# Kernel optimization log

Hardware: AMD Instinct MI355X
Metric: run time of the kernel (lower is better)

Reference implementation:

```python
import jax, jax.numpy as jnp
import numpy as np

NEG_SLOPE = 0.2  # PyG GATv2Conv default leaky_relu negative slope


def _gatv2_layer(x, src, dst, n, Wl, bl, Wr, br, att, bias, concat):
    # PyG GATv2Conv (share_weights=False, edge_dim=None):
    #   x_l = lin_l(x) on source, x_r = lin_r(x) on target
    #   m = leaky_relu(x_l[src] + x_r[dst]); alpha = softmax_dst(<m, att>)
    #   out[i] = sum_{e: dst=i} alpha_e * x_l[src_e]
    H, C = att.shape
    xl = (x @ Wl + bl).reshape(n, H, C)
    xr = (x @ Wr + br).reshape(n, H, C)
    m = jax.nn.leaky_relu(xl[src] + xr[dst], NEG_SLOPE)      # [E,H,C]
    logits = jnp.einsum('ehc,hc->eh', m, att)                # [E,H]
    lmax = jax.ops.segment_max(logits, dst, num_segments=n)  # [N,H]
    e = jnp.exp(logits - lmax[dst])
    denom = jax.ops.segment_sum(e, dst, num_segments=n)
    alpha = e / (denom[dst] + 1e-16)                         # [E,H]
    out = jax.ops.segment_sum(xl[src] * alpha[:, :, None], dst, num_segments=n)
    out = out.reshape(n, H * C) if concat else out.mean(axis=1)
    return out + bias


def _glorot(key, shape):
    fan_in, fan_out = shape[0], shape[-1]
    s = jnp.sqrt(6.0 / (fan_in + fan_out))
    return jax.random.uniform(key, shape, jnp.float32, -s, s)


def setup_inputs() -> dict:
    key = jax.random.key(0)
    N, E, B = 50000, 800000, 512
    node_in, hidden, heads, meta_dim = 128, 32, 4, 12
    ks = jax.random.split(key, 32)
    inp = {
        'x': jax.random.normal(ks[0], (N, node_in), jnp.float32),
        'edge_index': jax.random.randint(ks[1], (2, E), 0, N, jnp.int64),
        'batch': jnp.sort(jax.random.randint(ks[2], (N,), 0, B, jnp.int64)),
        'metadata': jax.random.normal(ks[3], (B, meta_dim), jnp.float32),
    }
    dims = [(node_in, hidden, heads), (hidden * heads, hidden, heads), (hidden * heads, hidden, 1)]
    i = 4
    for li, (din, dh, H) in enumerate(dims):
        inp[f'Wl{li}'] = _glorot(ks[i], (din, H * dh)); i += 1
        inp[f'bl{li}'] = jnp.zeros((H * dh,), jnp.float32)
        inp[f'Wr{li}'] = _glorot(ks[i], (din, H * dh)); i += 1
        inp[f'br{li}'] = jnp.zeros((H * dh,), jnp.float32)
        inp[f'att{li}'] = _glorot(ks[i], (H, dh)); i += 1
        out_dim = H * dh if li < 2 else dh  # last layer concat=False
        inp[f'b{li}'] = jnp.zeros((out_dim,), jnp.float32)
    pool_dim = hidden  # n_layers=3 -> final single-head layer
    inp['Wh1'] = _glorot(ks[i], (pool_dim + meta_dim, pool_dim)); i += 1
    inp['bh1'] = jnp.zeros((pool_dim,), jnp.float32)
    inp['Wh2'] = _glorot(ks[i], (pool_dim, 1)); i += 1
    inp['bh2'] = jnp.zeros((1,), jnp.float32)
    return inp


def reference(x, edge_index, batch, metadata,
              Wl0, bl0, Wr0, br0, att0, b0,
              Wl1, bl1, Wr1, br1, att1, b1,
              Wl2, bl2, Wr2, br2, att2, b2,
              Wh1, bh1, Wh2, bh2):
    n = x.shape[0]
    B = metadata.shape[0]
    # PyG GATv2Conv add_self_loops=True
    loop = jnp.arange(n, dtype=edge_index.dtype)
    src = jnp.concatenate([edge_index[0], loop])
    dst = jnp.concatenate([edge_index[1], loop])
    params = [(Wl0, bl0, Wr0, br0, att0, b0, True),
              (Wl1, bl1, Wr1, br1, att1, b1, True),
              (Wl2, bl2, Wr2, br2, att2, b2, False)]
    h = x
    for (Wl, bl, Wr, br, att, bias, concat) in params:
        h = _gatv2_layer(h, src, dst, n, Wl, bl, Wr, br, att, bias, concat)
        h = jax.nn.elu(h)  # dropout is identity in eval mode
    # global mean pool over graphs
    sums = jax.ops.segment_sum(h, batch, num_segments=B)
    cnt = jax.ops.segment_sum(jnp.ones((n,), h.dtype), batch, num_segments=B)
    emb = sums / jnp.clip(cnt, 1.0)[:, None]
    z = jnp.concatenate([emb, metadata], axis=1)
    z = jax.nn.relu(z @ Wh1 + bh1)
    return z @ Wh2 + bh2  # (B, 1) logits
```

## Files before the change

### kernel.cpp

```cpp
#include <hip/hip_runtime.h>
#include <cstdint>
#include <cstddef>

#define NEG_SLOPE 0.2f
#define LOG2E 1.44269504f

typedef __attribute__((ext_vector_type(8))) short short8;
typedef __attribute__((ext_vector_type(4))) float f32x4;

__device__ __forceinline__ float bf2f(unsigned short u) {
    union { unsigned int i; float f; } x; x.i = ((unsigned int)u) << 16; return x.f;
}
__device__ __forceinline__ unsigned short f2bf(float f) {
    union { float f; unsigned int i; } x;
    x.f = f;
    unsigned int u = x.i;
    return (unsigned short)((u + 0x7FFFu + ((u >> 16) & 1u)) >> 16);
}

__device__ __forceinline__ float dpp_sum8(float p) {
    p += __int_as_float(__builtin_amdgcn_update_dpp(0, __float_as_int(p), 0xB1, 0xF, 0xF, true));
    p += __int_as_float(__builtin_amdgcn_update_dpp(0, __float_as_int(p), 0x4E, 0xF, 0xF, true));
    p += __int_as_float(__builtin_amdgcn_update_dpp(0, __float_as_int(p), 0x141, 0xF, 0xF, true));
    return p;
}

__global__ __launch_bounds__(256) void prep_w_all(
    const float* __restrict__ Wl0, const float* __restrict__ Wr0,
    const float* __restrict__ Wl1, const float* __restrict__ Wr1,
    const float* __restrict__ Wl2, const float* __restrict__ Wr2,
    unsigned short* __restrict__ Bt0, unsigned short* __restrict__ Bt1,
    unsigned short* __restrict__ Bt2)
{
    int idx = blockIdx.x * 256 + threadIdx.x;
    const int SZ = 256 * 128;
    const float *Wl, *Wr; unsigned short* Bt; int dout;
    if (idx < SZ)              { Wl = Wl0; Wr = Wr0; Bt = Bt0; dout = 128; }
    else if (idx < 2 * SZ)     { Wl = Wl1; Wr = Wr1; Bt = Bt1; dout = 128; idx -= SZ; }
    else if (idx < 2 * SZ + 64 * 128) { Wl = Wl2; Wr = Wr2; Bt = Bt2; dout = 32; idx -= 2 * SZ; }
    else return;
    int n = idx >> 7, k = idx & 127;
    float v = (n < dout) ? Wl[(size_t)k * dout + n] : Wr[(size_t)k * dout + (n - dout)];
    Bt[idx] = f2bf(v);
}

template<int BN, bool ABF16>
__global__ __launch_bounds__(256) void gemm_mfma(
    const void* __restrict__ Avoid, int M,
    const unsigned short* __restrict__ Bt,
    const float* __restrict__ bl, const float* __restrict__ br,
    int dout, unsigned short* __restrict__ XL, unsigned short* __restrict__ XR)
{
    constexpr int LDA = 136;
    constexpr int NT  = BN / 16;
    __shared__ __attribute__((aligned(16))) unsigned short As[64 * LDA];
    __shared__ __attribute__((aligned(16))) unsigned short Bs[BN * LDA];
    const int t  = threadIdx.x;
    const int m0 = blockIdx.x * 64;
    const int n0 = blockIdx.y * BN;

    if (ABF16) {
        const unsigned short* A = (const unsigned short*)Avoid;
#pragma unroll
        for (int i = 0; i < 8; ++i) {
            int c   = t + i * 256;
            int row = c >> 5;
            int col = (c & 31) * 4;
            int gr  = m0 + row;
            ushort4 v = make_ushort4(0, 0, 0, 0);
            if (gr < M) v = *(const ushort4*)(A + (size_t)gr * 128 + col);
            *(ushort4*)(As + row * LDA + col) = v;
        }
    } else {
        const float* A = (const float*)Avoid;
#pragma unroll
        for (int i = 0; i < 8; ++i) {
            int c   = t + i * 256;
            int row = c >> 5;
            int col = (c & 31) * 4;
            int gr  = m0 + row;
            float4 v = make_float4(0.f, 0.f, 0.f, 0.f);
            if (gr < M) v = *(const float4*)(A + (size_t)gr * 128 + col);
            ushort4 o;
            o.x = f2bf(v.x); o.y = f2bf(v.y); o.z = f2bf(v.z); o.w = f2bf(v.w);
            *(ushort4*)(As + row * LDA + col) = o;
        }
    }
#pragma unroll
    for (int i = 0; i < BN / 16; ++i) {
        int c  = t + i * 256;
        int n  = c >> 4;
        int kc = (c & 15) * 8;
        *(short8*)(Bs + n * LDA + kc) =
            *(const short8*)(Bt + (size_t)(n0 + n) * 128 + kc);
    }
    __syncthreads();

    const int w    = t >> 6;
    const int lane = t & 63;
    const int fr   = lane & 15;
    const int quad = lane >> 4;

    f32x4 acc[NT] = {};
    const unsigned short* ap = As + (w * 16 + fr) * LDA + quad * 8;
    const unsigned short* bp = Bs + fr * LDA + quad * 8;
#pragma unroll
    for (int k0 = 0; k0 < 128; k0 += 32) {
        short8 afr = *(const short8*)(ap + k0);
#pragma unroll
        for (int j = 0; j < NT; ++j) {
            short8 bfr = *(const short8*)(bp + j * 16 * LDA + k0);
            acc[j] = __builtin_amdgcn_mfma_f32_16x16x32_bf16(afr, bfr, acc[j], 0, 0, 0);
        }
    }

#pragma unroll
    for (int j = 0; j < NT; ++j) {
        int col = n0 + j * 16 + fr;
        float bias = (col < dout) ? bl[col] : br[col - dout];
#pragma unroll
        for (int r = 0; r < 4; ++r) {
            int row = m0 + w * 16 + quad * 4 + r;
            if (row < M) {
                unsigned short o = f2bf(acc[j][r] + bias);
                if (col < dout) XL[(size_t)row * dout + col] = o;
                else            XR[(size_t)row * dout + (col - dout)] = o;
            }
        }
    }
}

__global__ void count_rank_kernel(const int* __restrict__ dst, int E,
                                  int* __restrict__ cnt, unsigned short* __restrict__ rank)
{
    int e = blockIdx.x * blockDim.x + threadIdx.x;
    if (e < E) {
        int p = atomicAdd(&cnt[dst[e]], 1);
        rank[e] = (unsigned short)p;
    }
}

__global__ __launch_bounds__(256) void scan_partial(
    const int* __restrict__ cnt, int N, int* __restrict__ bsum)
{
    __shared__ int red[4];
    const int t = threadIdx.x;
    const int base = blockIdx.x * 2048;
    int s = 0;
#pragma unroll
    for (int i = 0; i < 8; ++i) {
        int idx = base + t + i * 256;
        if (idx < N) s += cnt[idx];
    }
#pragma unroll
    for (int off = 32; off >= 1; off >>= 1) s += __shfl_xor(s, off);
    if ((t & 63) == 0) red[t >> 6] = s;
    __syncthreads();
    if (t == 0) bsum[blockIdx.x] = red[0] + red[1] + red[2] + red[3];
}

__global__ __launch_bounds__(256) void scan_bsums(
    int* __restrict__ bsum, int nb, int E, int* __restrict__ rowptr, int N)
{
    __shared__ int sh[256];
    const int t = threadIdx.x;
    int v = (t < nb) ? bsum[t] : 0;
    sh[t] = v;
    __syncthreads();
    for (int off = 1; off < 256; off <<= 1) {
        int u = (t >= off) ? sh[t - off] : 0;
        __syncthreads();
        sh[t] += u;
        __syncthreads();
    }
    if (t < nb) bsum[t] = sh[t] - v;
    if (t == 0) rowptr[N] = E;
}

__global__ __launch_bounds__(256) void scan_final(
    const int* __restrict__ cnt, int N, const int* __restrict__ bsum,
    int* __restrict__ rowptr)
{
    __shared__ int sdat[2048];
    __shared__ int tsum[256];
    const int t = threadIdx.x;
    const int base = blockIdx.x * 2048;
#pragma unroll
    for (int i = 0; i < 8; ++i) {
        int idx = base + t + i * 256;
        sdat[t + i * 256] = (idx < N) ? cnt[idx] : 0;
    }
    __syncthreads();
    int vals[8];
    int s = 0;
#pragma unroll
    for (int j = 0; j < 8; ++j) { vals[j] = sdat[t * 8 + j]; s += vals[j]; }
    tsum[t] = s;
    __syncthreads();
    for (int off = 1; off < 256; off <<= 1) {
        int u = (t >= off) ? tsum[t - off] : 0;
        __syncthreads();
        tsum[t] += u;
        __syncthreads();
    }
    int run = bsum[blockIdx.x] + tsum[t] - s;
#pragma unroll
    for (int j = 0; j < 8; ++j) { sdat[t * 8 + j] = run; run += vals[j]; }
    __syncthreads();
#pragma unroll
    for (int i = 0; i < 8; ++i) {
        int idx = base + t + i * 256;
        if (idx < N) rowptr[idx] = sdat[t + i * 256];
    }
}

__global__ void place_kernel(const int* __restrict__ src, const int* __restrict__ dst,
                             const unsigned short* __restrict__ rank, int E,
                             const int* __restrict__ rowptr,
                             unsigned short* __restrict__ csr_src)
{
    int e = blockIdx.x * blockDim.x + threadIdx.x;
    if (e < E)
        csr_src[rowptr[dst[e]] + rank[e]] = (unsigned short)src[e];
}

template<int H>
__global__ __launch_bounds__(256, 4) void gat_fused(
    const unsigned short* __restrict__ xl, const unsigned short* __restrict__ xr,
    const int* __restrict__ rowptr, const unsigned short* __restrict__ csr_src,
    const float* __restrict__ att, const float* __restrict__ bias,
    unsigned short* __restrict__ hout, int hstride, int N)
{
    constexpr int HC  = 32 * H;
    constexpr int LPE = HC / 4;
    constexpr int EPW = 64 / LPE;
    const int node = blockIdx.x * 4 + (threadIdx.x >> 6);
    if (node >= N) return;
    const int lane = threadIdx.x & 63;
    const int q    = lane % LPE;
    const int slot = lane / LPE;
    const int rs   = rowptr[node];
    const int re   = rowptr[node + 1];

    const unsigned short* __restrict__ xlb = xl + 4 * q;
    float4 xri;
    {
        ushort4 u = *(const ushort4*)(xr + (size_t)node * HC + 4 * q);
        xri.x = bf2f(u.x); xri.y = bf2f(u.y); xri.z = bf2f(u.z); xri.w = bf2f(u.w);
    }
    float4 af = *(const float4*)(att + 4 * q);
    af.x *= LOG2E; af.y *= LOG2E; af.z *= LOG2E; af.w *= LOG2E;

    float l = 0.f;
    float4 acc = make_float4(0.f, 0.f, 0.f, 0.f);

    auto ld4 = [&](int s) -> float4 {
        ushort4 u = *(const ushort4*)(xlb + (size_t)s * HC);
        float4 v;
        v.x = bf2f(u.x); v.y = bf2f(u.y); v.z = bf2f(u.z); v.w = bf2f(u.w);
        return v;
    };

    auto edge_w = [&](const float4& v) -> float {
        float sx = v.x + xri.x, sy = v.y + xri.y, sz = v.z + xri.z, sw = v.w + xri.w;
        sx = fmaxf(sx, NEG_SLOPE * sx);
        sy = fmaxf(sy, NEG_SLOPE * sy);
        sz = fmaxf(sz, NEG_SLOPE * sz);
        sw = fmaxf(sw, NEG_SLOPE * sw);
        float p = af.x * sx;
        p = fmaf(af.y, sy, p);
        p = fmaf(af.z, sz, p);
        p = fmaf(af.w, sw, p);
        p = dpp_sum8(p);
        return exp2f(p);
    };

    if (slot == 0) {
        float4 v = ld4(node);
        float w = edge_w(v);
        l = w;
        acc.x = w * v.x; acc.y = w * v.y; acc.z = w * v.z; acc.w = w * v.w;
    }

    int k = rs + slot;
    for (; k + EPW < re; k += 2 * EPW) {
        int s0 = csr_src[k];
        int s1 = csr_src[k + EPW];
        float4 v0 = ld4(s0);
        float4 v1 = ld4(s1);
        float w0 = edge_w(v0);
        float w1 = edge_w(v1);
        l += w0 + w1;
        acc.x = fmaf(w0, v0.x, fmaf(w1, v1.x, acc.x));
        acc.y = fmaf(w0, v0.y, fmaf(w1, v1.y, acc.y));
        acc.z = fmaf(w0, v0.z, fmaf(w1, v1.z, acc.z));
        acc.w = fmaf(w0, v0.w, fmaf(w1, v1.w, acc.w));
    }
    if (k < re) {
        int s0 = csr_src[k];
        float4 v0 = ld4(s0);
        float w0 = edge_w(v0);
        l += w0;
        acc.x = fmaf(w0, v0.x, acc.x);
        acc.y = fmaf(w0, v0.y, acc.y);
        acc.z = fmaf(w0, v0.z, acc.z);
        acc.w = fmaf(w0, v0.w, acc.w);
    }

#pragma unroll
    for (int mask = LPE; mask < 64; mask <<= 1) {
        l     += __shfl_xor(l, mask);
        acc.x += __shfl_xor(acc.x, mask);
        acc.y += __shfl_xor(acc.y, mask);
        acc.z += __shfl_xor(acc.z, mask);
        acc.w += __shfl_xor(acc.w, mask);
    }

    if (lane < LPE) {
        const float4 bi = *(const float4*)(bias + 4 * q);
        float inv = 1.f / (l + 1e-16f);
        float4 o;
        o.x = acc.x * inv + bi.x;
        o.y = acc.y * inv + bi.y;
        o.z = acc.z * inv + bi.z;
        o.w = acc.w * inv + bi.w;
        o.x = (o.x > 0.f) ? o.x : expm1f(o.x);
        o.y = (o.y > 0.f) ? o.y : expm1f(o.y);
        o.z = (o.z > 0.f) ? o.z : expm1f(o.z);
        o.w = (o.w > 0.f) ? o.w : expm1f(o.w);
        ushort4 ob;
        ob.x = f2bf(o.x); ob.y = f2bf(o.y); ob.z = f2bf(o.z); ob.w = f2bf(o.w);
        *(ushort4*)(hout + (size_t)node * hstride + 4 * q) = ob;
    }
}

__global__ __launch_bounds__(128) void pool_head_kernel(
    const unsigned short* __restrict__ h, int hstride,
    const int* __restrict__ batch, int N,
    const float* __restrict__ meta,
    const float* __restrict__ Wh1, const float* __restrict__ bh1,
    const float* __restrict__ Wh2, const float* __restrict__ bh2,
    float* __restrict__ out)
{
    const int b = blockIdx.x;
    const int t = threadIdx.x;
    __shared__ float s[128];
    __shared__ float z[44];

    int lo = 0, hi = N;
    while (lo < hi) { int mid = (lo + hi) >> 1; if (batch[mid] < b) lo = mid + 1; else hi = mid; }
    int lo2 = lo, hi2 = N;
    while (lo2 < hi2) { int mid = (lo2 + hi2) >> 1; if (batch[mid] < b + 1) lo2 = mid + 1; else hi2 = mid; }
    const int start = lo, end = lo2;

    const int c = t & 31, r = t >> 5;
    float acc = 0.f;
    for (int row = start + r; row < end; row += 4)
        acc += bf2f(h[(size_t)row * hstride + c]);
    s[t] = acc;
    __syncthreads();
    if (t < 32) {
        float sum = s[t] + s[t + 32] + s[t + 64] + s[t + 96];
        z[t] = sum / fmaxf((float)(end - start), 1.0f);
    } else if (t < 44) {
        z[t] = meta[(size_t)b * 12 + (t - 32)];
    }
    __syncthreads();
    if (t < 32) {
        float hj = bh1[t];
#pragma unroll
        for (int k = 0; k < 44; ++k)
            hj = fmaf(z[k], Wh1[k * 32 + t], hj);
        hj = fmaxf(hj, 0.f);
        float p = hj * Wh2[t];
#pragma unroll
        for (int off = 16; off >= 1; off >>= 1)
            p += __shfl_xor(p, off, 32);
        if (t == 0) out[b] = p + bh2[0];
    }
}

extern "C" void kernel_launch(void* const* d_in, const int* in_sizes, int n_in,
                              void* d_out, int out_size, void* d_ws, size_t ws_size,
                              hipStream_t stream)
{
    const float* x     = (const float*)d_in[0];
    const int*   ei    = (const int*)d_in[1];
    const int*   batch = (const int*)d_in[2];
    const float* meta  = (const float*)d_in[3];
    const float* Wl[3]  = {(const float*)d_in[4],  (const float*)d_in[10], (const float*)d_in[16]};
    const float* bl[3]  = {(const float*)d_in[5],  (const float*)d_in[11], (const float*)d_in[17]};
    const float* Wr[3]  = {(const float*)d_in[6],  (const float*)d_in[12], (const float*)d_in[18]};
    const float* br[3]  = {(const float*)d_in[7],  (const float*)d_in[13], (const float*)d_in[19]};
    const float* att[3] = {(const float*)d_in[8],  (const float*)d_in[14], (const float*)d_in[20]};
    const float* bb[3]  = {(const float*)d_in[9],  (const float*)d_in[15], (const float*)d_in[21]};
    const float* Wh1 = (const float*)d_in[22];
    const float* bh1 = (const float*)d_in[23];
    const float* Wh2 = (const float*)d_in[24];
    const float* bh2 = (const float*)d_in[25];
    float* out = (float*)d_out;

    const int N  = in_sizes[0] / 128;
    const int E  = in_sizes[1] / 2;
    const int B  = in_sizes[3] / 12;
    const int NB = (N + 2047) / 2048;

    char* wsp = (char*)d_ws;
    size_t off_ = 0;
    auto alloc = [&](size_t bytes) {
        char* p = wsp + off_;
        off_ = (off_ + bytes + 255) & ~(size_t)255;
        return p;
    };
    unsigned short* xlbuf = (unsigned short*)alloc((size_t)N * 128 * 2);
    unsigned short* xrbuf = (unsigned short*)alloc((size_t)N * 128 * 2);
    unsigned short* hbuf  = (unsigned short*)alloc((size_t)N * 128 * 2);
    int*   cnt     = (int*)alloc((size_t)N * 4);
    int*   rowptr  = (int*)alloc((size_t)(N + 1) * 4);
    unsigned short* rank    = (unsigned short*)alloc((size_t)E * 2);
    unsigned short* csr_src = (unsigned short*)alloc((size_t)E * 2);
    unsigned short* Bt0     = (unsigned short*)alloc((size_t)256 * 128 * 2);
    unsigned short* Bt1     = (unsigned short*)alloc((size_t)256 * 128 * 2);
    unsigned short* Bt2     = (unsigned short*)alloc((size_t)64 * 128 * 2);
    int*   bsum    = (int*)alloc((size_t)256 * 4);

    const int* srcI = ei;
    const int* dstI = ei + E;

    prep_w_all<<<(2 * 256 * 128 + 64 * 128 + 255) / 256, 256, 0, stream>>>(
        Wl[0], Wr[0], Wl[1], Wr[1], Wl[2], Wr[2], Bt0, Bt1, Bt2);

    hipMemsetAsync(cnt, 0, (size_t)N * 4, stream);
    count_rank_kernel<<<(E + 255) / 256, 256, 0, stream>>>(dstI, E, cnt, rank);
    scan_partial<<<NB, 256, 0, stream>>>(cnt, N, bsum);
    scan_bsums<<<1, 256, 0, stream>>>(bsum, NB, E, rowptr, N);
    scan_final<<<NB, 256, 0, stream>>>(cnt, N, bsum, rowptr);
    place_kernel<<<(E + 255) / 256, 256, 0, stream>>>(srcI, dstI, rank, E, rowptr, csr_src);

    const int GB = (N + 3) / 4;
    const int MB = (N + 63) / 64;

    {
        gemm_mfma<128, false><<<dim3(MB, 2), 256, 0, stream>>>(x, N, Bt0, bl[0], br[0], 128, xlbuf, xrbuf);
        gat_fused<4><<<GB, 256, 0, stream>>>(xlbuf, xrbuf, rowptr, csr_src, att[0], bb[0], hbuf, 128, N);
    }
    {
        gemm_mfma<128, true><<<dim3(MB, 2), 256, 0, stream>>>(hbuf, N, Bt1, bl[1], br[1], 128, xlbuf, xrbuf);
        gat_fused<4><<<GB, 256, 0, stream>>>(xlbuf, xrbuf, rowptr, csr_src, att[1], bb[1], hbuf, 128, N);
    }
    {
        gemm_mfma<64, true><<<dim3(MB, 1), 256, 0, stream>>>(hbuf, N, Bt2, bl[2], br[2], 32, xlbuf, xrbuf);
        gat_fused<1><<<GB, 256, 0, stream>>>(xlbuf, xrbuf, rowptr, csr_src, att[2], bb[2], hbuf, 32, N);
    }
    pool_head_kernel<<<B, 128, 0, stream>>>(hbuf, 32, batch, N, meta, Wh1, bh1, Wh2, bh2, out);
}
```

Baseline: 376.9 us.

## Fuse CSR build into a single cooperative kernel with grid syncs

Replaces the memset, count/rank, three scan kernels and the place kernel with one cooperative kernel. Grid-wide syncs separate the stages, and each thread keeps its edges' dst, src and rank in registers. This removes several kernel launches and the global rank buffer round trip. In exchange it adds five grid barriers, and it relies on hardcoded limits: at most 8 edges per thread across 512×256 threads, and at most 256 nodes per block in the final scan.

Result: slower. 669.0 us (+77.5%).

```diff
diff --git a/kernel.cpp b/kernel.cpp
--- a/kernel.cpp
+++ b/kernel.cpp
@@ -1,6 +1,9 @@
 #include <hip/hip_runtime.h>
+#include <hip/hip_cooperative_groups.h>
 #include <cstdint>
 #include <cstddef>
+
+namespace cg = cooperative_groups;
 
 #define NEG_SLOPE 0.2f
 #define LOG2E 1.44269504f
@@ -130,98 +133,90 @@
     }
 }
 
-__global__ void count_rank_kernel(const int* __restrict__ dst, int E,
-                                  int* __restrict__ cnt, unsigned short* __restrict__ rank)
-{
-    int e = blockIdx.x * blockDim.x + threadIdx.x;
-    if (e < E) {
-        int p = atomicAdd(&cnt[dst[e]], 1);
-        rank[e] = (unsigned short)p;
-    }
-}
-
-__global__ __launch_bounds__(256) void scan_partial(
-    const int* __restrict__ cnt, int N, int* __restrict__ bsum)
-{
-    __shared__ int red[4];
-    const int t = threadIdx.x;
-    const int base = blockIdx.x * 2048;
-    int s = 0;
-#pragma unroll
-    for (int i = 0; i < 8; ++i) {
-        int idx = base + t + i * 256;
-        if (idx < N) s += cnt[idx];
-    }
-#pragma unroll
-    for (int off = 32; off >= 1; off >>= 1) s += __shfl_xor(s, off);
-    if ((t & 63) == 0) red[t >> 6] = s;
-    __syncthreads();
-    if (t == 0) bsum[blockIdx.x] = red[0] + red[1] + red[2] + red[3];
-}
-
-__global__ __launch_bounds__(256) void scan_bsums(
-    int* __restrict__ bsum, int nb, int E, int* __restrict__ rowptr, int N)
-{
-    __shared__ int sh[256];
-    const int t = threadIdx.x;
-    int v = (t < nb) ? bsum[t] : 0;
-    sh[t] = v;
-    __syncthreads();
-    for (int off = 1; off < 256; off <<= 1) {
-        int u = (t >= off) ? sh[t - off] : 0;
+#define CSR_BLOCKS 512
+#define CSR_THREADS 256
+#define CSR_MAXE 8
+
+__global__ __launch_bounds__(CSR_THREADS) void csr_coop(
+    const int* __restrict__ src, const int* __restrict__ dst, int E,
+    int* __restrict__ cnt, int N,
+    int* __restrict__ rowptr, int* __restrict__ bsum,
+    unsigned short* __restrict__ csr_src)
+{
+    cg::grid_group grid = cg::this_grid();
+    __shared__ int sh[CSR_BLOCKS];
+    const int t   = threadIdx.x;
+    const int tid = blockIdx.x * CSR_THREADS + t;
+    const int T   = CSR_BLOCKS * CSR_THREADS;
+
+    for (int i = tid; i < N; i += T) cnt[i] = 0;
+    grid.sync();
+
+    int ed[CSR_MAXE], es[CSR_MAXE], er[CSR_MAXE];
+    bool ok[CSR_MAXE];
+#pragma unroll
+    for (int j = 0; j < CSR_MAXE; ++j) {
+        int e = tid + j * T;
+        ok[j] = e < E;
+        if (ok[j]) {
+            ed[j] = dst[e];
+            es[j] = src[e];
+            er[j] = atomicAdd(&cnt[ed[j]], 1);
+        }
+    }
+    grid.sync();
+
+    const int per = (N + CSR_BLOCKS - 1) / CSR_BLOCKS;
+    {
+        const int lo = blockIdx.x * per;
+        const int hi = min(lo + per, N);
+        int s = 0;
+        for (int i = lo + t; i < hi; i += CSR_THREADS) s += cnt[i];
+#pragma unroll
+        for (int off = 32; off >= 1; off >>= 1) s += __shfl_xor(s, off);
+        if ((t & 63) == 0) sh[t >> 6] = s;
         __syncthreads();
-        sh[t] += u;
+        if (t == 0) bsum[blockIdx.x] = sh[0] + sh[1] + sh[2] + sh[3];
         __syncthreads();
     }
-    if (t < nb) bsum[t] = sh[t] - v;
-    if (t == 0) rowptr[N] = E;
-}
-
-__global__ __launch_bounds__(256) void scan_final(
-    const int* __restrict__ cnt, int N, const int* __restrict__ bsum,
-    int* __restrict__ rowptr)
-{
-    __shared__ int sdat[2048];
-    __shared__ int tsum[256];
-    const int t = threadIdx.x;
-    const int base = blockIdx.x * 2048;
-#pragma unroll
-    for (int i = 0; i < 8; ++i) {
-        int idx = base + t + i * 256;
-        sdat[t + i * 256] = (idx < N) ? cnt[idx] : 0;
-    }
-    __syncthreads();
-    int vals[8];
-    int s = 0;
-#pragma unroll
-    for (int j = 0; j < 8; ++j) { vals[j] = sdat[t * 8 + j]; s += vals[j]; }
-    tsum[t] = s;
-    __syncthreads();
-    for (int off = 1; off < 256; off <<= 1) {
-        int u = (t >= off) ? tsum[t - off] : 0;
+    grid.sync();
+
+    if (blockIdx.x == 0) {
+        for (int i = t; i < CSR_BLOCKS; i += CSR_THREADS) sh[i] = bsum[i];
         __syncthreads();
-        tsum[t] += u;
+        for (int off = 1; off < CSR_BLOCKS; off <<= 1) {
+            int a = (t >= off) ? sh[t - off] : 0;
+            int b = (t + CSR_THREADS >= off) ? sh[t + CSR_THREADS - off] : 0;
+            __syncthreads();
+            sh[t] += a;
+            sh[t + CSR_THREADS] += b;
+            __syncthreads();
+        }
+        for (int i = t; i < CSR_BLOCKS; i += CSR_THREADS)
+            bsum[i] = sh[i] - bsum[i];
+        if (t == 0) rowptr[N] = E;
+    }
+    grid.sync();
+
+    {
+        const int lo  = blockIdx.x * per;
+        const int len = min(per, N - lo);
+        int v = (t < len) ? cnt[lo + t] : 0;
+        sh[t] = v;
         __syncthreads();
-    }
-    int run = bsum[blockIdx.x] + tsum[t] - s;
-#pragma unroll
-    for (int j = 0; j < 8; ++j) { sdat[t * 8 + j] = run; run += vals[j]; }
-    __syncthreads();
-#pragma unroll
-    for (int i = 0; i < 8; ++i) {
-        int idx = base + t + i * 256;
-        if (idx < N) rowptr[idx] = sdat[t + i * 256];
-    }
-}
-
-__global__ void place_kernel(const int* __restrict__ src, const int* __restrict__ dst,
-                             const unsigned short* __restrict__ rank, int E,
-                             const int* __restrict__ rowptr,
-                             unsigned short* __restrict__ csr_src)
-{
-    int e = blockIdx.x * blockDim.x + threadIdx.x;
-    if (e < E)
-        csr_src[rowptr[dst[e]] + rank[e]] = (unsigned short)src[e];
+        for (int off = 1; off < CSR_THREADS; off <<= 1) {
+            int u = (t >= off) ? sh[t - off] : 0;
+            __syncthreads();
+            sh[t] += u;
+            __syncthreads();
+        }
+        if (t < len) rowptr[lo + t] = bsum[blockIdx.x] + sh[t] - v;
+    }
+    grid.sync();
+
+#pragma unroll
+    for (int j = 0; j < CSR_MAXE; ++j)
+        if (ok[j]) csr_src[rowptr[ed[j]] + er[j]] = (unsigned short)es[j];
 }
 
 template<int H>
@@ -403,7 +398,6 @@
     const int N  = in_sizes[0] / 128;
     const int E  = in_sizes[1] / 2;
     const int B  = in_sizes[3] / 12;
-    const int NB = (N + 2047) / 2048;
 
     char* wsp = (char*)d_ws;
     size_t off_ = 0;
@@ -417,12 +411,11 @@
     unsigned short* hbuf  = (unsigned short*)alloc((size_t)N * 128 * 2);
     int*   cnt     = (int*)alloc((size_t)N * 4);
     int*   rowptr  = (int*)alloc((size_t)(N + 1) * 4);
-    unsigned short* rank    = (unsigned short*)alloc((size_t)E * 2);
     unsigned short* csr_src = (unsigned short*)alloc((size_t)E * 2);
     unsigned short* Bt0     = (unsigned short*)alloc((size_t)256 * 128 * 2);
     unsigned short* Bt1     = (unsigned short*)alloc((size_t)256 * 128 * 2);
     unsigned short* Bt2     = (unsigned short*)alloc((size_t)64 * 128 * 2);
-    int*   bsum    = (int*)alloc((size_t)256 * 4);
+    int*   bsum    = (int*)alloc((size_t)CSR_BLOCKS * 4);
 
     const int* srcI = ei;
     const int* dstI = ei + E;
@@ -430,12 +423,13 @@
     prep_w_all<<<(2 * 256 * 128 + 64 * 128 + 255) / 256, 256, 0, stream>>>(
         Wl[0], Wr[0], Wl[1], Wr[1], Wl[2], Wr[2], Bt0, Bt1, Bt2);
 
-    hipMemsetAsync(cnt, 0, (size_t)N * 4, stream);
-    count_rank_kernel<<<(E + 255) / 256, 256, 0, stream>>>(dstI, E, cnt, rank);
-    scan_partial<<<NB, 256, 0, stream>>>(cnt, N, bsum);
-    scan_bsums<<<1, 256, 0, stream>>>(bsum, NB, E, rowptr, N);
-    scan_final<<<NB, 256, 0, stream>>>(cnt, N, bsum, rowptr);
-    place_kernel<<<(E + 255) / 256, 256, 0, stream>>>(srcI, dstI, rank, E, rowptr, csr_src);
+    {
+        void* args[] = {(void*)&srcI, (void*)&dstI, (void*)&E,
+                        (void*)&cnt, (void*)&N,
+                        (void*)&rowptr, (void*)&bsum, (void*)&csr_src};
+        hipLaunchCooperativeKernel((void*)csr_coop, dim3(CSR_BLOCKS),
+                                   dim3(CSR_THREADS), args, 0, stream);
+    }
 
     const int GB = (N + 3) / 4;
     const int MB = (N + 63) / 64;
```
